# Kernel tuning notes

Hardware: AMD Instinct MI355X
Metric: run time of the kernel (lower is better)

Reference implementation:

```python
import jax, jax.numpy as jnp
import numpy as np
import math

ALPHA = 0.25
GAMMA = 2.0
STD = np.array([0.1, 0.1, 0.2, 0.2], dtype=np.float32).reshape(4, 1)


def setup_inputs() -> dict:
    rng = np.random.default_rng(0)
    B, C, Na, Nb = 8, 80, 49104, 64
    cls_pred = rng.uniform(0.01, 0.99, (B, C, Na)).astype(np.float32)
    reg_pred = (0.5 * rng.standard_normal((B, 4, Na))).astype(np.float32)
    # anchors in x1,y1,x2,y2 with positive width/height
    cx = rng.uniform(0.0, 512.0, Na); cy = rng.uniform(0.0, 512.0, Na)
    w = rng.uniform(16.0, 128.0, Na); h = rng.uniform(16.0, 128.0, Na)
    anchors = np.stack([cx - 0.5 * w, cy - 0.5 * h, cx + 0.5 * w, cy + 0.5 * h], 1).astype(np.float32)
    # annotations: valid boxes first, padded with label=-1
    x1 = rng.uniform(0.0, 380.0, (B, Nb)); y1 = rng.uniform(0.0, 380.0, (B, Nb))
    bw = rng.uniform(24.0, 120.0, (B, Nb)); bh = rng.uniform(24.0, 120.0, (B, Nb))
    lab = rng.integers(0, C, (B, Nb)).astype(np.float32)
    nvalid = rng.integers(1, Nb + 1, B)
    valid = np.arange(Nb)[None, :] < nvalid[:, None]
    lab = np.where(valid, lab, -1.0)
    annots = np.stack([x1, y1, x1 + bw, y1 + bh, lab], -1).astype(np.float32)
    return {"cls_pred": jnp.asarray(cls_pred), "reg_pred": jnp.asarray(reg_pred),
            "annots": jnp.asarray(annots), "anchors": jnp.asarray(anchors)}


def _focal(pred, targets):
    alpha_f = jnp.where(targets == 1.0, ALPHA, 1.0 - ALPHA)
    fw = jnp.where(targets == 1.0, 1.0 - pred, pred)
    bce = -(targets * jnp.log(pred) + (1.0 - targets) * jnp.log(1.0 - pred))
    return alpha_f * fw ** GAMMA * bce


def _ciou(acx, acy, aw, ah, gcx, gcy, gw, gh, reg):
    # acx/acy/aw/ah: [1,Na]; gt: [B,Na]; reg: [B,4,Na] (std-scaled)
    pcx = acx + reg[:, 0] * aw
    pcy = acy + reg[:, 1] * ah
    pw = jnp.exp(reg[:, 2]) * aw
    ph = jnp.exp(reg[:, 3]) * ah
    g_area = gw * gh
    p_area = pw * ph
    ix1 = jnp.maximum(gcx - 0.5 * gw, pcx - 0.5 * pw)
    ix2 = jnp.minimum(gcx + 0.5 * gw, pcx + 0.5 * pw)
    iy1 = jnp.maximum(gcy - 0.5 * gh, pcy - 0.5 * ph)
    iy2 = jnp.minimum(gcy + 0.5 * gh, pcy + 0.5 * ph)
    inter = jnp.clip(ix2 - ix1, 0.0) * jnp.clip(iy2 - iy1, 0.0)
    ex1 = jnp.minimum(gcx - 0.5 * gw, pcx - 0.5 * pw)
    ex2 = jnp.maximum(gcx + 0.5 * gw, pcx + 0.5 * pw)
    ey1 = jnp.minimum(gcy - 0.5 * gh, pcy - 0.5 * ph)
    ey2 = jnp.maximum(gcy + 0.5 * gh, pcy + 0.5 * ph)
    inter_diag = (gcx - pcx) ** 2 + (gcy - pcy) ** 2
    enc_diag = jnp.clip(ex2 - ex1, 0.0) ** 2 + jnp.clip(ey2 - ey1, 0.0) ** 2
    union = g_area + p_area - inter
    u = inter_diag / jnp.clip(enc_diag, 1e-6)
    iou = inter / jnp.clip(union, 1e-6)
    v = (4.0 / math.pi ** 2) * (jnp.arctan(gw / gh) - jnp.arctan(pw / ph)) ** 2
    S = (iou > 0.5).astype(iou.dtype)
    alpha = jax.lax.stop_gradient(S * v / jnp.clip(1.0 - iou + v, 1e-6))
    ciou = jnp.clip(iou - u - alpha * v, -1.0, 1.0)
    return 1.0 - ciou


def _multibox_loss(cls_pred, reg_pred, annots, anchors):
    reg = reg_pred * jnp.asarray(STD)[None]            # [B,4,Na]
    aw = anchors[:, 2] - anchors[:, 0]
    ah = anchors[:, 3] - anchors[:, 1]
    acx = anchors[:, 0] + 0.5 * aw
    acy = anchors[:, 1] + 0.5 * ah
    cls = jnp.clip(cls_pred, 1e-7, 1.0 - 1e-7)         # [B,C,Na]
    valid = annots[:, :, 4] != -1.0                    # [B,Nb]
    boxes = annots[:, :, :4]
    # dense IoU [B,Na,Nb]
    a = anchors[None, :, None, :]
    bx = boxes[:, None, :, :]
    a_area = aw * ah                                   # [Na]
    b_area = (boxes[..., 2] - boxes[..., 0]) * (boxes[..., 3] - boxes[..., 1])
    iw = jnp.clip(jnp.minimum(a[..., 2], bx[..., 2]) - jnp.maximum(a[..., 0], bx[..., 0]), 0.0)
    ih = jnp.clip(jnp.minimum(a[..., 3], bx[..., 3]) - jnp.maximum(a[..., 1], bx[..., 1]), 0.0)
    inter = iw * ih
    union = jnp.clip(a_area[None, :, None] + b_area[:, None, :] - inter, 1e-7)
    iou = inter / union
    iou = jnp.where(valid[:, None, :], iou, -1.0)      # mask padded boxes
    iou_max = iou.max(-1)                              # [B,Na]
    iou_arg = iou.argmax(-1)                           # [B,Na]
    has_boxes = valid.any(-1)                          # [B]
    pos = (iou_max >= 0.5) & has_boxes[:, None]        # [B,Na]
    assigned = jnp.take_along_axis(annots, iou_arg[..., None], axis=1)  # [B,Na,5]
    labels = assigned[..., 4].astype(jnp.int32)
    C = cls.shape[1]
    posf = pos.astype(cls.dtype)
    targets = jax.nn.one_hot(labels, C, dtype=cls.dtype) * posf[..., None]
    targets = jnp.transpose(targets, (0, 2, 1))        # [B,C,Na]
    num_pos = posf.sum(-1)                             # [B]
    cls_loss = _focal(cls, targets).sum((1, 2)) / jnp.clip(num_pos, 1.0)
    gw = jnp.clip(assigned[..., 2] - assigned[..., 0], 1.0)
    gh = jnp.clip(assigned[..., 3] - assigned[..., 1], 1.0)
    gcx = assigned[..., 0] + 0.5 * gw
    gcy = assigned[..., 1] + 0.5 * gh
    ciou = _ciou(acx[None], acy[None], aw[None], ah[None], gcx, gcy, gw, gh, reg)  # [B,Na]
    reg_loss = (ciou * posf).sum(-1) / jnp.clip(num_pos, 1.0)
    reg_loss = jnp.where(num_pos > 0, reg_loss, 0.0)
    return cls_loss.mean(), reg_loss.mean()


def reference(cls_pred, reg_pred, annots, anchors):
    return _multibox_loss(cls_pred, reg_pred, annots, anchors)
```

## Files before the change

kernel.cpp:

```cpp
#include <hip/hip_runtime.h>
#include <math.h>

#define NB_MAX 64
#define CCHUNK 20


__global__ void zero_kernel(float* acc) {
    if (threadIdx.x < 32) acc[threadIdx.x] = 0.f;
}

__global__ __launch_bounds__(256) void assign_kernel(
    const float* __restrict__ reg_pred,
    const float* __restrict__ annots,
    const float* __restrict__ anchors,
    signed char* __restrict__ labels,
    float* __restrict__ accum,
    int Na, int Nb)
{
    int b = blockIdx.y;
    int a = blockIdx.x * 256 + threadIdx.x;

    __shared__ float ann[NB_MAX][5];
    const float* ab = annots + b * Nb * 5;
    for (int i = threadIdx.x; i < Nb * 5; i += 256) ann[i / 5][i % 5] = ab[i];
    __syncthreads();

    float regv = 0.f, posv = 0.f;
    if (a < Na) {
        float4 anc = ((const float4*)anchors)[a];
        float ax1 = anc.x, ay1 = anc.y, ax2 = anc.z, ay2 = anc.w;
        float aw = ax2 - ax1, ah = ay2 - ay1;
        float a_area = aw * ah;

        float best = -1.f; int bestj = 0;
        for (int j = 0; j < Nb; ++j) {
            float lab = ann[j][4];
            float iou = -1.0f;
            if (lab != -1.0f) {
                float bx1 = ann[j][0], by1 = ann[j][1], bx2 = ann[j][2], by2 = ann[j][3];
                float iw = fmaxf(fminf(ax2, bx2) - fmaxf(ax1, bx1), 0.f);
                float ih = fmaxf(fminf(ay2, by2) - fmaxf(ay1, by1), 0.f);
                float inter = iw * ih;
                float b_area = (bx2 - bx1) * (by2 - by1);
                float un = fmaxf(a_area + b_area - inter, 1e-7f);
                iou = inter / un;
            }
            if (iou > best) { best = iou; bestj = j; }
        }

        signed char lout = -1;
        if (best >= 0.5f) {
            lout = (signed char)(int)ann[bestj][4];

            float r0 = reg_pred[(size_t)(b * 4 + 0) * Na + a] * 0.1f;
            float r1 = reg_pred[(size_t)(b * 4 + 1) * Na + a] * 0.1f;
            float r2 = reg_pred[(size_t)(b * 4 + 2) * Na + a] * 0.2f;
            float r3 = reg_pred[(size_t)(b * 4 + 3) * Na + a] * 0.2f;

            float acx = ax1 + 0.5f * aw, acy = ay1 + 0.5f * ah;
            float pcx = acx + r0 * aw;
            float pcy = acy + r1 * ah;
            float pw = expf(r2) * aw;
            float ph = expf(r3) * ah;

            float g0 = ann[bestj][0], g1 = ann[bestj][1];
            float g2 = ann[bestj][2], g3 = ann[bestj][3];
            float gw = fmaxf(g2 - g0, 1.0f);
            float gh = fmaxf(g3 - g1, 1.0f);
            float gcx = g0 + 0.5f * gw;
            float gcy = g1 + 0.5f * gh;

            float g_area = gw * gh, p_area = pw * ph;
            float ix1 = fmaxf(gcx - 0.5f * gw, pcx - 0.5f * pw);
            float ix2 = fminf(gcx + 0.5f * gw, pcx + 0.5f * pw);
            float iy1 = fmaxf(gcy - 0.5f * gh, pcy - 0.5f * ph);
            float iy2 = fminf(gcy + 0.5f * gh, pcy + 0.5f * ph);
            float inter = fmaxf(ix2 - ix1, 0.f) * fmaxf(iy2 - iy1, 0.f);

            float ex1 = fminf(gcx - 0.5f * gw, pcx - 0.5f * pw);
            float ex2 = fmaxf(gcx + 0.5f * gw, pcx + 0.5f * pw);
            float ey1 = fminf(gcy - 0.5f * gh, pcy - 0.5f * ph);
            float ey2 = fmaxf(gcy + 0.5f * gh, pcy + 0.5f * ph);

            float dx = gcx - pcx, dy = gcy - pcy;
            float inter_diag = dx * dx + dy * dy;
            float cdx = fmaxf(ex2 - ex1, 0.f), cdy = fmaxf(ey2 - ey1, 0.f);
            float enc_diag = cdx * cdx + cdy * cdy;

            float uni = g_area + p_area - inter;
            float u = inter_diag / fmaxf(enc_diag, 1e-6f);
            float iou = inter / fmaxf(uni, 1e-6f);
            float dv = atanf(gw / gh) - atanf(pw / ph);
            float v = (4.0f / (float)(M_PI * M_PI)) * dv * dv;
            float S = (iou > 0.5f) ? 1.f : 0.f;
            float alpha = S * v / fmaxf(1.f - iou + v, 1e-6f);
            float ciou = fminf(fmaxf(iou - u - alpha * v, -1.f), 1.f);
            regv = 1.f - ciou;
            posv = 1.f;
        }
        labels[(size_t)b * Na + a] = lout;
    }

    __shared__ float s1[4], s2[4];
    #pragma unroll
    for (int off = 32; off > 0; off >>= 1) {
        regv += __shfl_down(regv, off);
        posv += __shfl_down(posv, off);
    }
    int lane = threadIdx.x & 63, wid = threadIdx.x >> 6;
    if (lane == 0) { s1[wid] = regv; s2[wid] = posv; }
    __syncthreads();
    if (threadIdx.x == 0) {
        float r = s1[0] + s1[1] + s1[2] + s1[3];
        float p = s2[0] + s2[1] + s2[2] + s2[3];
        atomicAdd(&accum[8 + b], r);
        atomicAdd(&accum[16 + b], p);
    }
}

__device__ __forceinline__ float focal1(float p, bool t) {
    p = fminf(fmaxf(p, 1e-7f), 0.99999988f);
    float q = t ? p : 1.0f - p;
    float af = t ? 0.25f : 0.75f;
    float fw = 1.0f - q;
    return af * fw * fw * (-__logf(q));
}

__global__ __launch_bounds__(256) void focal_kernel(
    const float* __restrict__ cls_pred,
    const signed char* __restrict__ labels,
    float* __restrict__ accum,
    int Na, int C)
{
    int b = blockIdx.z;
    int Nq = Na >> 2;
    int q = blockIdx.x * 256 + threadIdx.x;
    int c0 = blockIdx.y * CCHUNK;
    int cend = min(c0 + CCHUNK, C);

    float sum = 0.f;
    if (q < Nq) {
        char4 lab = ((const char4*)labels)[(size_t)b * Nq + q];
        int l0 = lab.x, l1 = lab.y, l2 = lab.z, l3 = lab.w;
        const float4* base = (const float4*)cls_pred + (size_t)b * C * Nq + q;
        for (int c = c0; c < cend; ++c) {
            float4 p = base[(size_t)c * Nq];
            sum += focal1(p.x, l0 == c);
            sum += focal1(p.y, l1 == c);
            sum += focal1(p.z, l2 == c);
            sum += focal1(p.w, l3 == c);
        }
    }

    __shared__ float s[4];
    #pragma unroll
    for (int off = 32; off > 0; off >>= 1) sum += __shfl_down(sum, off);
    int lane = threadIdx.x & 63, wid = threadIdx.x >> 6;
    if (lane == 0) s[wid] = sum;
    __syncthreads();
    if (threadIdx.x == 0) {
        atomicAdd(&accum[b], s[0] + s[1] + s[2] + s[3]);
    }
}

__global__ void finalize_kernel(const float* __restrict__ accum,
                                float* __restrict__ out, int B)
{
    if (threadIdx.x == 0) {
        float cs = 0.f, rs = 0.f;
        for (int b = 0; b < B; ++b) {
            float npv = accum[16 + b];
            float d = fmaxf(npv, 1.f);
            cs += accum[b] / d;
            rs += (npv > 0.f) ? accum[8 + b] / d : 0.f;
        }
        out[0] = cs / (float)B;
        out[1] = rs / (float)B;
    }
}

extern "C" void kernel_launch(void* const* d_in, const int* in_sizes, int n_in,
                              void* d_out, int out_size, void* d_ws, size_t ws_size,
                              hipStream_t stream) {
    const float* cls     = (const float*)d_in[0];
    const float* reg     = (const float*)d_in[1];
    const float* annots  = (const float*)d_in[2];
    const float* anchors = (const float*)d_in[3];

    int Na = in_sizes[3] / 4;
    int B  = in_sizes[1] / (4 * Na);
    int C  = in_sizes[0] / (B * Na);
    int Nb = in_sizes[2] / (B * 5);

    float* accum = (float*)d_ws;
    signed char* labels = (signed char*)d_ws + 256;
    float* out = (float*)d_out;

    zero_kernel<<<1, 64, 0, stream>>>(accum);

    dim3 g1((Na + 255) / 256, B);
    assign_kernel<<<g1, 256, 0, stream>>>(reg, annots, anchors, labels, accum, Na, Nb);

    int Nq = Na / 4;
    dim3 g2((Nq + 255) / 256, (C + CCHUNK - 1) / CCHUNK, B);
    focal_kernel<<<g2, 256, 0, stream>>>(cls, labels, accum, Na, C);

    finalize_kernel<<<1, 64, 0, stream>>>(accum, out, B);
}
```

Measured before the change: 230.2 us.

## Replace atomic accumulation with per-block partials and widen focal per-thread work

Removes the zero kernel and the global atomicAdds. Each block now writes its partial sums to a workspace slot, and a 512-thread finalize kernel reduces those slots per batch. The focal kernel now gives each thread 8 anchors (two float4 loads) instead of 4, and CCHUNK drops from 20 to 10, so the grid changes shape and each thread has more loads in flight. The gains are one fewer launch, no atomic contention and a deterministic sum; the cost is extra partial-buffer traffic and a heavier finalize pass.

Result: faster. 210.7 us (-8.5%).

```diff
diff --git a/kernel.cpp b/kernel.cpp
--- a/kernel.cpp
+++ b/kernel.cpp
@@ -2,20 +2,17 @@
 #include <math.h>
 
 #define NB_MAX 64
-#define CCHUNK 20
-
-
-__global__ void zero_kernel(float* acc) {
-    if (threadIdx.x < 32) acc[threadIdx.x] = 0.f;
-}
+#define CCHUNK 10
+
 
 __global__ __launch_bounds__(256) void assign_kernel(
     const float* __restrict__ reg_pred,
     const float* __restrict__ annots,
     const float* __restrict__ anchors,
     signed char* __restrict__ labels,
-    float* __restrict__ accum,
-    int Na, int Nb)
+    float* __restrict__ reg_part,
+    float* __restrict__ pos_part,
+    int Na, int Nb, int nblkA)
 {
     int b = blockIdx.y;
     int a = blockIdx.x * 256 + threadIdx.x;
@@ -111,10 +108,8 @@
     if (lane == 0) { s1[wid] = regv; s2[wid] = posv; }
     __syncthreads();
     if (threadIdx.x == 0) {
-        float r = s1[0] + s1[1] + s1[2] + s1[3];
-        float p = s2[0] + s2[1] + s2[2] + s2[3];
-        atomicAdd(&accum[8 + b], r);
-        atomicAdd(&accum[16 + b], p);
+        reg_part[(size_t)b * nblkA + blockIdx.x] = s1[0] + s1[1] + s1[2] + s1[3];
+        pos_part[(size_t)b * nblkA + blockIdx.x] = s2[0] + s2[1] + s2[2] + s2[3];
     }
 }
 
@@ -129,26 +124,34 @@
 __global__ __launch_bounds__(256) void focal_kernel(
     const float* __restrict__ cls_pred,
     const signed char* __restrict__ labels,
-    float* __restrict__ accum,
-    int Na, int C)
+    float* __restrict__ cls_part,
+    int Na, int C, int nchunk, int nblkF)
 {
     int b = blockIdx.z;
+    int No = Na >> 3;
     int Nq = Na >> 2;
     int q = blockIdx.x * 256 + threadIdx.x;
     int c0 = blockIdx.y * CCHUNK;
     int cend = min(c0 + CCHUNK, C);
 
     float sum = 0.f;
-    if (q < Nq) {
-        char4 lab = ((const char4*)labels)[(size_t)b * Nq + q];
-        int l0 = lab.x, l1 = lab.y, l2 = lab.z, l3 = lab.w;
-        const float4* base = (const float4*)cls_pred + (size_t)b * C * Nq + q;
+    if (q < No) {
+        const char4* lp = (const char4*)(labels + (size_t)b * Na) + 2 * q;
+        char4 la = lp[0], lb = lp[1];
+        int l0 = la.x, l1 = la.y, l2 = la.z, l3 = la.w;
+        int l4 = lb.x, l5 = lb.y, l6 = lb.z, l7 = lb.w;
+        const float4* base = (const float4*)cls_pred + (size_t)b * C * Nq + 2 * q;
         for (int c = c0; c < cend; ++c) {
-            float4 p = base[(size_t)c * Nq];
-            sum += focal1(p.x, l0 == c);
-            sum += focal1(p.y, l1 == c);
-            sum += focal1(p.z, l2 == c);
-            sum += focal1(p.w, l3 == c);
+            float4 p0 = base[(size_t)c * Nq];
+            float4 p1 = base[(size_t)c * Nq + 1];
+            sum += focal1(p0.x, l0 == c);
+            sum += focal1(p0.y, l1 == c);
+            sum += focal1(p0.z, l2 == c);
+            sum += focal1(p0.w, l3 == c);
+            sum += focal1(p1.x, l4 == c);
+            sum += focal1(p1.y, l5 == c);
+            sum += focal1(p1.z, l6 == c);
+            sum += focal1(p1.w, l7 == c);
         }
     }
 
@@ -159,23 +162,49 @@
     if (lane == 0) s[wid] = sum;
     __syncthreads();
     if (threadIdx.x == 0) {
-        atomicAdd(&accum[b], s[0] + s[1] + s[2] + s[3]);
-    }
-}
-
-__global__ void finalize_kernel(const float* __restrict__ accum,
-                                float* __restrict__ out, int B)
+        cls_part[(size_t)b * nblkF + blockIdx.x * nchunk + blockIdx.y] =
+            s[0] + s[1] + s[2] + s[3];
+    }
+}
+
+__global__ __launch_bounds__(512) void finalize_kernel(
+    const float* __restrict__ reg_part,
+    const float* __restrict__ pos_part,
+    const float* __restrict__ cls_part,
+    float* __restrict__ out,
+    int B, int nblkA, int nblkF)
 {
+    int w = threadIdx.x >> 6;
+    int lane = threadIdx.x & 63;
+
+    float cs = 0.f, rs = 0.f, ps = 0.f;
+    if (w < B) {
+        for (int i = lane; i < nblkA; i += 64) {
+            rs += reg_part[(size_t)w * nblkA + i];
+            ps += pos_part[(size_t)w * nblkA + i];
+        }
+        for (int i = lane; i < nblkF; i += 64) {
+            cs += cls_part[(size_t)w * nblkF + i];
+        }
+    }
+    #pragma unroll
+    for (int off = 32; off > 0; off >>= 1) {
+        cs += __shfl_down(cs, off);
+        rs += __shfl_down(rs, off);
+        ps += __shfl_down(ps, off);
+    }
+    __shared__ float sc[8], sr[8];
+    if (w < B && lane == 0) {
+        float d = fmaxf(ps, 1.f);
+        sc[w] = cs / d;
+        sr[w] = (ps > 0.f) ? rs / d : 0.f;
+    }
+    __syncthreads();
     if (threadIdx.x == 0) {
-        float cs = 0.f, rs = 0.f;
-        for (int b = 0; b < B; ++b) {
-            float npv = accum[16 + b];
-            float d = fmaxf(npv, 1.f);
-            cs += accum[b] / d;
-            rs += (npv > 0.f) ? accum[8 + b] / d : 0.f;
-        }
-        out[0] = cs / (float)B;
-        out[1] = rs / (float)B;
+        float a = 0.f, r = 0.f;
+        for (int i = 0; i < B; ++i) { a += sc[i]; r += sr[i]; }
+        out[0] = a / (float)B;
+        out[1] = r / (float)B;
     }
 }
 
@@ -192,18 +221,26 @@
     int C  = in_sizes[0] / (B * Na);
     int Nb = in_sizes[2] / (B * 5);
 
-    float* accum = (float*)d_ws;
-    signed char* labels = (signed char*)d_ws + 256;
+    int nblkA  = (Na + 255) / 256;
+    int No     = Na / 8;
+    int nblkX  = (No + 255) / 256;
+    int nchunk = (C + CCHUNK - 1) / CCHUNK;
+    int nblkF  = nblkX * nchunk;
+
+    signed char* labels = (signed char*)d_ws;
+    size_t off = ((size_t)B * Na + 255) & ~(size_t)255;
+    float* reg_part = (float*)((char*)d_ws + off);
+    float* pos_part = reg_part + (size_t)B * nblkA;
+    float* cls_part = pos_part + (size_t)B * nblkA;
     float* out = (float*)d_out;
 
-    zero_kernel<<<1, 64, 0, stream>>>(accum);
-
-    dim3 g1((Na + 255) / 256, B);
-    assign_kernel<<<g1, 256, 0, stream>>>(reg, annots, anchors, labels, accum, Na, Nb);
-
-    int Nq = Na / 4;
-    dim3 g2((Nq + 255) / 256, (C + CCHUNK - 1) / CCHUNK, B);
-    focal_kernel<<<g2, 256, 0, stream>>>(cls, labels, accum, Na, C);
-
-    finalize_kernel<<<1, 64, 0, stream>>>(accum, out, B);
-}
+    dim3 g1(nblkA, B);
+    assign_kernel<<<g1, 256, 0, stream>>>(reg, annots, anchors, labels,
+                                          reg_part, pos_part, Na, Nb, nblkA);
+
+    dim3 g2(nblkX, nchunk, B);
+    focal_kernel<<<g2, 256, 0, stream>>>(cls, labels, cls_part, Na, C, nchunk, nblkF);
+
+    finalize_kernel<<<1, 512, 0, stream>>>(reg_part, pos_part, cls_part, out,
+                                           B, nblkA, nblkF);
+}
```
